# Optimization experiments

Measured on AMD Instinct MI355X. Metric: run time of the kernel, lower is better.

The kernel has to match this reference:

```python
import jax, jax.numpy as jnp
import numpy as np

B, N, D, H, HD = 4, 2048, 512, 8, 64
FF = 1024
C2, HF, WF = 128, 64, 64
EPS = 1e-6


def setup_inputs() -> dict:
    key = jax.random.key(0)
    ks = jax.random.split(key, 9)
    def nrm(k, shape, s=0.02):
        return jax.random.normal(k, shape, dtype=jnp.float32) * s
    x = jax.random.normal(ks[0], (B, N, D), dtype=jnp.float32)
    theta = jax.random.normal(ks[1], (B, H, N, HD // 2), dtype=jnp.float32)
    fmaps = jax.random.normal(ks[2], (B, C2, HF, WF), dtype=jnp.float32)
    # pixel-unit (x, y) coords in [0, W-1] / [0, H-1]
    coords = jax.random.uniform(ks[3], (B, N, 2), dtype=jnp.float32) * (WF - 1)
    return dict(
        x=x, theta=theta, fmaps=fmaps, coords=coords,
        w_corr=nrm(ks[4], (D, C2)),
        norm1_scale=jnp.ones((D,), jnp.float32),
        qk_scale_q=jnp.ones((HD,), jnp.float32),
        qk_scale_k=jnp.ones((HD,), jnp.float32),
        w_qkv=nrm(ks[5], (3 * D, D)),
        w_out=nrm(ks[6], (D, D)),
        norm2_scale=jnp.ones((D,), jnp.float32),
        w_ff1=nrm(ks[7], (2 * FF, D)),
        b_ff1=jnp.zeros((2 * FF,), jnp.float32),
        w_ff2=nrm(ks[8], (D, FF)),
    )


def rms_norm(x, scale, eps=EPS):
    ms = jnp.mean(jnp.square(x), axis=-1, keepdims=True)
    return x * (scale * jax.lax.rsqrt(ms + eps))


def apply_rotary(x, theta):
    # rotates first 2*d channels of the head dim, as in _apply_rotary_emb_inplace
    d = theta.shape[-1]
    x1, x2 = x[..., :d], x[..., d:2 * d]
    cos, sin = jnp.cos(theta), jnp.sin(theta)
    y1 = x1 * cos - x2 * sin
    y2 = x2 * cos + x1 * sin
    return jnp.concatenate([y1, y2, x[..., 2 * d:]], axis=-1)


def bilinear_sample(fmaps, coords):
    # fmaps [B,C,H,W], coords [B,N,2] (x,y) pixels; border padding, align_corners=True
    Hh, Ww = fmaps.shape[-2], fmaps.shape[-1]
    xc = jnp.clip(coords[..., 0], 0.0, Ww - 1.0)
    yc = jnp.clip(coords[..., 1], 0.0, Hh - 1.0)
    x0 = jnp.floor(xc); y0 = jnp.floor(yc)
    wx = xc - x0; wy = yc - y0
    x0i = x0.astype(jnp.int32); x1i = jnp.minimum(x0i + 1, Ww - 1)
    y0i = y0.astype(jnp.int32); y1i = jnp.minimum(y0i + 1, Hh - 1)
    def gather_one(img, yi, xi):  # img [C,H,W] -> [C,N]
        return img[:, yi, xi]
    g = jax.vmap(gather_one)
    f00 = g(fmaps, y0i, x0i); f01 = g(fmaps, y0i, x1i)
    f10 = g(fmaps, y1i, x0i); f11 = g(fmaps, y1i, x1i)
    wx = wx[:, None, :]; wy = wy[:, None, :]
    top = f00 * (1.0 - wx) + f01 * wx
    bot = f10 * (1.0 - wx) + f11 * wx
    out = top * (1.0 - wy) + bot * wy  # [B,C,N]
    return jnp.transpose(out, (0, 2, 1))  # [B,N,C]


def reference(x, theta, fmaps, coords, w_corr, norm1_scale, qk_scale_q,
              qk_scale_k, w_qkv, w_out, norm2_scale, w_ff1, b_ff1, w_ff2):
    # correlation features injected into tokens
    feats = bilinear_sample(fmaps, coords)          # [B,N,C2]
    x = x + feats @ w_corr.T                        # [B,N,D]
    # --- attention block (pre-RMSNorm, qk-norm, RoPE, unscaled dot-product attn) ---
    skip = x
    xn = rms_norm(x, norm1_scale)
    qkv = xn @ w_qkv.T                              # [B,N,3D]
    q, k, v = jnp.split(qkv, 3, axis=-1)
    def to_heads(t):
        return jnp.transpose(t.reshape(t.shape[0], t.shape[1], H, HD), (0, 2, 1, 3))
    q, k, v = to_heads(q), to_heads(k), to_heads(v)  # [B,H,N,HD]
    q = rms_norm(q, qk_scale_q)
    k = rms_norm(k, qk_scale_k)
    q = apply_rotary(q, theta)
    k = apply_rotary(k, theta)
    # dot_product_attn: raw q @ k^T (no 1/sqrt(d)), softmax, @ v
    attn = jax.nn.softmax(jnp.einsum('bhid,bhjd->bhij', q, k), axis=-1)
    o = jnp.einsum('bhij,bhjd->bhid', attn, v)
    o = jnp.transpose(o, (0, 2, 1, 3)).reshape(x.shape[0], x.shape[1], D)
    x = skip + o @ w_out.T
    # --- feedforward block (GEGLU) ---
    skip = x
    xn = rms_norm(x, norm2_scale)
    h = xn @ w_ff1.T + b_ff1
    hx, gate = jnp.split(h, 2, axis=-1)
    h = hx * jax.nn.gelu(gate, approximate=False)
    return skip + h @ w_ff2.T
```

## Files before the change

### kernel.cpp

```cpp
#include <hip/hip_runtime.h>
#include <hip/hip_bf16.h>
#include <math.h>

#define Bsz 4
#define Nseq 2048
#define Dm 512
#define Hn 8
#define HDm 64
#define FFm 1024
#define Cc 128
#define EPSf 1e-6f

typedef __attribute__((ext_vector_type(8))) short short8;
typedef __attribute__((ext_vector_type(4))) float f32x4;
typedef __attribute__((ext_vector_type(16))) float f32x16;
typedef __attribute__((ext_vector_type(4))) unsigned u32x4;

#define AS1(p) ((__attribute__((address_space(1))) void*)((void*)(p)))
#define AS3(p) ((__attribute__((address_space(3))) void*)(p))

__device__ __forceinline__ float bf2f(unsigned short u) {
    return __uint_as_float(((unsigned)u) << 16);
}
__device__ __forceinline__ unsigned short f2bf(float f) {
    unsigned u = __float_as_uint(f);
    return (unsigned short)((u + 0x7fffu + ((u >> 16) & 1u)) >> 16);
}
__device__ __forceinline__ unsigned cvt_pk_bf16(float lo, float hi) {
    unsigned r;
    asm("v_cvt_pk_bf16_f32 %0, %1, %2" : "=v"(r) : "v"(lo), "v"(hi));
    return r;
}
__device__ __forceinline__ bool is_f32(const unsigned* dtp) {
    return dtp[0] == 0x3F800000u;
}

#define LOG2E 1.4426950408889634f
#define SHIFT2 92.33248261689366f

#define CONV_TOTAL 2690176
__global__ __launch_bounds__(256) void convert_kernel(
    const void* s0, const void* s1, const void* s2, const void* s3,
    const void* s4, const void* s5, const void* s6, const void* s7,
    const void* s8, const void* s9,
    unsigned short* __restrict__ canon, const unsigned* __restrict__ dtp)
{
    int i = blockIdx.x * 256 + threadIdx.x;
    if (i >= CONV_TOTAL) return;
    const void* src; int j;
    if      (i < 786432)  { src = s0; j = i; }
    else if (i < 1835008) { src = s1; j = i - 786432; }
    else if (i < 2359296) { src = s2; j = i - 1835008; }
    else if (i < 2621440) { src = s3; j = i - 2359296; }
    else if (i < 2686976) { src = s4; j = i - 2621440; }
    else if (i < 2689024) { src = s5; j = i - 2686976; }
    else if (i < 2689536) { src = s6; j = i - 2689024; }
    else if (i < 2690048) { src = s7; j = i - 2689536; }
    else if (i < 2690112) { src = s8; j = i - 2690048; }
    else                  { src = s9; j = i - 2690112; }
    canon[i] = is_f32(dtp) ? f2bf(((const float*)src)[j])
                           : ((const unsigned short*)src)[j];
}

__global__ __launch_bounds__(256) void sample_kernel(
    const void* __restrict__ fmaps,
    const void* __restrict__ coords,
    unsigned short* __restrict__ feats,
    const unsigned* __restrict__ dtp)
{
    const bool f32m = is_f32(dtp);
    int i = blockIdx.x * 256 + threadIdx.x;
    int t = i >> 7;
    int c = i & 127;
    int b = t >> 11;
    float xc, yc;
    if (f32m) { xc = ((const float*)coords)[2 * t];  yc = ((const float*)coords)[2 * t + 1]; }
    else      { xc = bf2f(((const unsigned short*)coords)[2 * t]);
                yc = bf2f(((const unsigned short*)coords)[2 * t + 1]); }
    xc = fminf(fmaxf(xc, 0.f), 63.f);
    yc = fminf(fmaxf(yc, 0.f), 63.f);
    float x0f = floorf(xc), y0f = floorf(yc);
    float wx = xc - x0f, wy = yc - y0f;
    int x0 = (int)x0f, y0 = (int)y0f;
    int x1 = min(x0 + 1, 63), y1 = min(y0 + 1, 63);
    size_t fb = ((size_t)b * Cc + c) << 12;
    float f00, f01, f10, f11;
    if (f32m) {
        const float* fp = (const float*)fmaps + fb;
        f00 = fp[(y0 << 6) + x0]; f01 = fp[(y0 << 6) + x1];
        f10 = fp[(y1 << 6) + x0]; f11 = fp[(y1 << 6) + x1];
    } else {
        const unsigned short* fp = (const unsigned short*)fmaps + fb;
        f00 = bf2f(fp[(y0 << 6) + x0]); f01 = bf2f(fp[(y0 << 6) + x1]);
        f10 = bf2f(fp[(y1 << 6) + x0]); f11 = bf2f(fp[(y1 << 6) + x1]);
    }
    float top = f00 * (1.f - wx) + f01 * wx;
    float bot = f10 * (1.f - wx) + f11 * wx;
    feats[i] = f2bf(top * (1.f - wy) + bot * wy);
}

template<int BN>
__global__ __launch_bounds__(256, 4) void gemm_bt(
    const unsigned short* __restrict__ A,
    const unsigned short* __restrict__ W,
    const unsigned short* __restrict__ bias,
    const float* __restrict__ resF,
    const void* __restrict__ resRaw,
    float* __restrict__ outF,
    unsigned short* __restrict__ outB,
    void* __restrict__ outRaw,
    const unsigned* __restrict__ dtp,
    int M, int N, int K)
{
    constexpr int NT = BN / 32;
    __shared__ __align__(16) unsigned short As[2][128 * 32];
    __shared__ __align__(16) unsigned short Bs[2][BN * 32];
    const int tid = threadIdx.x;
    const int wave = tid >> 6, lane = tid & 63;
    const int quad = lane >> 4, l16 = lane & 15;
    const int wm = wave >> 1, wn = wave & 1;
    const int rowBase = blockIdx.y * 128;
    const int colBase = blockIdx.x * BN;
    const unsigned short* Ab = A + (size_t)rowBase * K;
    const unsigned short* Wb = W + (size_t)colBase * K;
    const int sr = lane >> 2;
    const int sc = (lane & 3) * 8;

    f32x4 acc[4][NT] = {};

    auto stage = [&](int buf, int k0) {
#pragma unroll
        for (int c = 0; c < 2; ++c) {
            int chunk = wave + c * 4;
            const unsigned short* ga = Ab + (size_t)(chunk * 16 + sr) * K + k0 + sc;
            __builtin_amdgcn_global_load_lds(AS1(ga), AS3(&As[buf][chunk * 512]), 16, 0, 0);
        }
#pragma unroll
        for (int c = 0; c < BN / 16; c += 4) {
            int chunk = wave + c;
            const unsigned short* gb = Wb + (size_t)(chunk * 16 + sr) * K + k0 + sc;
            __builtin_amdgcn_global_load_lds(AS1(gb), AS3(&Bs[buf][chunk * 512]), 16, 0, 0);
        }
    };

    const int nk = K >> 5;
    stage(0, 0);
    for (int kt = 0; kt < nk; ++kt) {
        const int buf = kt & 1;
        __syncthreads();
        __builtin_amdgcn_sched_barrier(0);
        if (kt + 1 < nk) stage(1 - buf, (kt + 1) << 5);
        short8 af[4], bfr[NT];
#pragma unroll
        for (int mt = 0; mt < 4; ++mt)
            af[mt] = *(const short8*)&As[buf][(wm * 64 + mt * 16 + l16) * 32 + quad * 8];
#pragma unroll
        for (int nt = 0; nt < NT; ++nt)
            bfr[nt] = *(const short8*)&Bs[buf][(wn * (BN / 2) + nt * 16 + l16) * 32 + quad * 8];
        __builtin_amdgcn_s_setprio(1);
#pragma unroll
        for (int mt = 0; mt < 4; ++mt)
#pragma unroll
            for (int nt = 0; nt < NT; ++nt)
                acc[mt][nt] = __builtin_amdgcn_mfma_f32_16x16x32_bf16(
                    af[mt], bfr[nt], acc[mt][nt], 0, 0, 0);
        __builtin_amdgcn_s_setprio(0);
    }

    const bool f32m = dtp ? is_f32(dtp) : false;
#pragma unroll
    for (int mt = 0; mt < 4; ++mt) {
#pragma unroll
        for (int r = 0; r < 4; ++r) {
            int row = rowBase + wm * 64 + mt * 16 + quad * 4 + r;
            size_t rowoff = (size_t)row * N;
#pragma unroll
            for (int nt = 0; nt < NT; ++nt) {
                int col = colBase + wn * (BN / 2) + nt * 16 + l16;
                float v = acc[mt][nt][r];
                if (bias) v += bf2f(bias[col]);
                size_t idx = rowoff + col;
                if (resF) v += resF[idx];
                if (resRaw) v += f32m ? ((const float*)resRaw)[idx]
                                      : bf2f(((const unsigned short*)resRaw)[idx]);
                if (outF)      outF[idx] = v;
                else if (outB) outB[idx] = f2bf(v);
                else if (f32m) ((float*)outRaw)[idx] = v;
                else           ((unsigned short*)outRaw)[idx] = f2bf(v);
            }
        }
    }
}

__global__ __launch_bounds__(256) void rmsnorm_kernel(
    const float* __restrict__ X, const unsigned short* __restrict__ scale,
    unsigned short* __restrict__ Y)
{
    int t = blockIdx.x;
    int tid = threadIdx.x;
    const float* xr = X + (size_t)t * 512;
    float a = xr[tid], b = xr[tid + 256];
    float ss = a * a + b * b;
#pragma unroll
    for (int off = 1; off < 64; off <<= 1) ss += __shfl_xor(ss, off);
    __shared__ float red[4];
    int wave = tid >> 6, lane = tid & 63;
    if (lane == 0) red[wave] = ss;
    __syncthreads();
    float tot = red[0] + red[1] + red[2] + red[3];
    float r = rsqrtf(tot * (1.f / 512.f) + EPSf);
    Y[(size_t)t * 512 + tid]       = f2bf(a * (bf2f(scale[tid]) * r));
    Y[(size_t)t * 512 + tid + 256] = f2bf(b * (bf2f(scale[tid + 256]) * r));
}

__global__ __launch_bounds__(256) void qkv_rope_kernel(
    const unsigned short* __restrict__ qkv, const void* __restrict__ theta,
    const unsigned short* __restrict__ sq, const unsigned short* __restrict__ sk,
    unsigned short* __restrict__ Qo, unsigned short* __restrict__ Ko,
    const unsigned* __restrict__ dtp)
{
    const bool f32m = is_f32(dtp);
    int t = blockIdx.x;
    int b = t >> 11, n = t & 2047;
    int wave = threadIdx.x >> 6, lane = threadIdx.x & 63;
    const unsigned short* base = qkv + (size_t)t * 1536;
#pragma unroll
    for (int hh = 0; hh < 2; ++hh) {
        int h = wave + hh * 4;
        float q = bf2f(base[h * 64 + lane]);
        float k = bf2f(base[512 + h * 64 + lane]);
        float ssq = q * q, ssk = k * k;
#pragma unroll
        for (int off = 1; off < 64; off <<= 1) {
            ssq += __shfl_xor(ssq, off);
            ssk += __shfl_xor(ssk, off);
        }
        float qn = q * (bf2f(sq[lane]) * rsqrtf(ssq * (1.f / 64.f) + EPSf));
        float kn = k * (bf2f(sk[lane]) * rsqrtf(ssk * (1.f / 64.f) + EPSf));
        size_t thIdx = ((size_t)(b * Hn + h) * Nseq + n) * 32 + (lane & 31);
        float th = f32m ? ((const float*)theta)[thIdx]
                        : bf2f(((const unsigned short*)theta)[thIdx]);
        float cth = __cosf(th), sth = __sinf(th);
        float qp = __shfl_xor(qn, 32);
        float kp = __shfl_xor(kn, 32);
        float sgn = (lane < 32) ? -1.f : 1.f;
        float qr = qn * cth + sgn * qp * sth;
        float kr = kn * cth + sgn * kp * sth;
        size_t o = ((size_t)(b * Hn + h) * Nseq + n) * 64 + lane;
        Qo[o] = f2bf(qr * LOG2E);
        Ko[o] = f2bf(kr);
    }
}

__global__ __launch_bounds__(256) void vtrans_kernel(
    const unsigned short* __restrict__ qkvb, unsigned short* __restrict__ Vt)
{
    int bh = blockIdx.y;
    int b = bh >> 3, h = bh & 7;
    int tid = threadIdx.x;
    int d = tid & 63;
    int chunk = blockIdx.x * 4 + (tid >> 6);
    int n0 = chunk * 8;
    unsigned short v[8];
#pragma unroll
    for (int j = 0; j < 8; ++j)
        v[j] = qkvb[((size_t)(b * Nseq + n0 + j)) * 1536 + 1024 + h * 64 + d];
    *(short8*)&Vt[((size_t)bh * 64 + d) * Nseq + n0] = *(short8*)v;
}

__global__ __launch_bounds__(256, 4) void attn_kernel(
    const unsigned short* __restrict__ Qg,
    const unsigned short* __restrict__ Kg,
    const unsigned short* __restrict__ Vtg,
    float* __restrict__ Op,
    float* __restrict__ Lp)
{
    const int bh = blockIdx.x;
    const int b = bh >> 3, h = bh & 7;
    const int q0 = blockIdx.y * 128;
    const int kz = blockIdx.z;
    const int tid = threadIdx.x;
    const int wave = tid >> 6, lane = tid & 63;
    const int l31 = lane & 31, hh = lane >> 5;
    __shared__ __align__(16) unsigned short Ks[2][64 * 72];
    __shared__ __align__(16) unsigned short Vs[2][64 * 72];
    const size_t bhN = (size_t)bh * Nseq;

    short8 bq[4];
#pragma unroll
    for (int kc = 0; kc < 4; ++kc)
        bq[kc] = *(const short8*)&Qg[(bhN + q0 + wave * 32 + l31) * 64 + kc * 16 + hh * 8];

    f32x16 oa[2] = {};
    float lsum = 0.f;
    const int r8 = tid >> 3;
    const int c8e = (tid & 7) * 8;
    const unsigned short* kgb = Kg + bhN * 64;
    const unsigned short* vbase = Vtg + (size_t)bh * 64 * Nseq;
    const bool hi = (hh == 1);

    const int KT0 = kz * (Nseq / 128);
    const int KT1 = KT0 + (Nseq / 128);
    const int kb0 = KT0 * 64;

    short8 kr0 = *(const short8*)&kgb[(size_t)(kb0 + r8) * 64 + c8e];
    short8 kr1 = *(const short8*)&kgb[(size_t)(kb0 + r8 + 32) * 64 + c8e];
    short8 vr0 = *(const short8*)&vbase[(size_t)r8 * Nseq + kb0 + c8e];
    short8 vr1 = *(const short8*)&vbase[(size_t)(r8 + 32) * Nseq + kb0 + c8e];

    for (int kt = KT0; kt < KT1; ++kt) {
        const int cur = kt & 1;
        *(short8*)&Ks[cur][r8 * 72 + c8e]        = kr0;
        *(short8*)&Ks[cur][(r8 + 32) * 72 + c8e] = kr1;
        *(short8*)&Vs[cur][r8 * 72 + c8e]        = vr0;
        *(short8*)&Vs[cur][(r8 + 32) * 72 + c8e] = vr1;
        __syncthreads();
        __builtin_amdgcn_sched_barrier(0);
        if (kt + 1 < KT1) {
            const int kb = (kt + 1) * 64;
            kr0 = *(const short8*)&kgb[(size_t)(kb + r8) * 64 + c8e];
            kr1 = *(const short8*)&kgb[(size_t)(kb + r8 + 32) * 64 + c8e];
            vr0 = *(const short8*)&vbase[(size_t)r8 * Nseq + kb + c8e];
            vr1 = *(const short8*)&vbase[(size_t)(r8 + 32) * Nseq + kb + c8e];
        }

        f32x16 st[2];
#pragma unroll
        for (int mt = 0; mt < 2; ++mt)
#pragma unroll
            for (int e = 0; e < 16; ++e) st[mt][e] = -SHIFT2;
        __builtin_amdgcn_s_setprio(1);
#pragma unroll
        for (int kc = 0; kc < 4; ++kc) {
            short8 ak0 = *(const short8*)&Ks[cur][(l31) * 72 + kc * 16 + hh * 8];
            short8 ak1 = *(const short8*)&Ks[cur][(32 + l31) * 72 + kc * 16 + hh * 8];
            st[0] = __builtin_amdgcn_mfma_f32_32x32x16_bf16(ak0, bq[kc], st[0], 0, 0, 0);
            st[1] = __builtin_amdgcn_mfma_f32_32x32x16_bf16(ak1, bq[kc], st[1], 0, 0, 0);
        }
        __builtin_amdgcn_s_setprio(0);

        unsigned pk[2][8];
        float partial = 0.f;
#pragma unroll
        for (int t = 0; t < 2; ++t)
#pragma unroll
            for (int p = 0; p < 4; ++p) {
                float v0 = __builtin_amdgcn_exp2f(st[t][4 * p + 0]);
                float v1 = __builtin_amdgcn_exp2f(st[t][4 * p + 1]);
                float v2 = __builtin_amdgcn_exp2f(st[t][4 * p + 2]);
                float v3 = __builtin_amdgcn_exp2f(st[t][4 * p + 3]);
                partial += (v0 + v1) + (v2 + v3);
                pk[t][2 * p + 0] = cvt_pk_bf16(v0, v1);
                pk[t][2 * p + 1] = cvt_pk_bf16(v2, v3);
            }
        lsum += partial + __shfl_xor(partial, 32);

        __builtin_amdgcn_s_setprio(1);
#pragma unroll
        for (int kc = 0; kc < 4; ++kc) {
            const int tau = kc >> 1;
            const int pA = 2 * (kc & 1);
            const int pB = pA + 1;
            unsigned dA0 = pk[tau][2 * pA], dA1 = pk[tau][2 * pA + 1];
            unsigned dB0 = pk[tau][2 * pB], dB1 = pk[tau][2 * pB + 1];
            unsigned s0 = hi ? dA0 : dB0, s1 = hi ? dA1 : dB1;
            unsigned r0 = __shfl_xor(s0, 32), r1 = __shfl_xor(s1, 32);
            unsigned o0 = hi ? dB0 : dA0, o1 = hi ? dB1 : dA1;
            u32x4 av = { hi ? r0 : o0, hi ? r1 : o1,
                         hi ? o0 : r0, hi ? o1 : r1 };
            short8 ap = __builtin_bit_cast(short8, av);
            short8 bv0 = *(const short8*)&Vs[cur][(l31) * 72 + kc * 16 + hh * 8];
            short8 bv1 = *(const short8*)&Vs[cur][(32 + l31) * 72 + kc * 16 + hh * 8];
            oa[0] = __builtin_amdgcn_mfma_f32_32x32x16_bf16(ap, bv0, oa[0], 0, 0, 0);
            oa[1] = __builtin_amdgcn_mfma_f32_32x32x16_bf16(ap, bv1, oa[1], 0, 0, 0);
        }
        __builtin_amdgcn_s_setprio(0);
    }

    if (!hi)
        Lp[((size_t)kz * 32 + bh) * Nseq + q0 + wave * 32 + l31] = lsum;
    const size_t obase = (size_t)kz * (Bsz * Nseq);
#pragma unroll
    for (int nt = 0; nt < 2; ++nt)
#pragma unroll
        for (int i = 0; i < 16; ++i) {
            int qr = q0 + wave * 32 + (i & 3) + 8 * (i >> 2) + 4 * hh;
            Op[(obase + (size_t)b * Nseq + qr) * Dm + h * 64 + nt * 32 + l31] =
                oa[nt][i];
        }
}

__global__ __launch_bounds__(256) void attn_combine_kernel(
    const float* __restrict__ Op,
    const float* __restrict__ Lp,
    unsigned short* __restrict__ Og)
{
    int gid = blockIdx.x * 256 + threadIdx.x;
    size_t base = (size_t)gid * 8;
    int t = gid >> 6;
    int c = (gid & 63) * 8;
    int h = c >> 6;
    int bh = ((t >> 11) << 3) + h;
    int n = t & 2047;
    float l = Lp[(size_t)bh * Nseq + n] + Lp[(size_t)(32 * Nseq) + (size_t)bh * Nseq + n];
    float inv = 1.f / l;
    f32x4 a0 = *(const f32x4*)&Op[base];
    f32x4 a1 = *(const f32x4*)&Op[base + 4];
    f32x4 b0 = *(const f32x4*)&Op[(size_t)8192 * 512 + base];
    f32x4 b1 = *(const f32x4*)&Op[(size_t)8192 * 512 + base + 4];
    unsigned short o[8];
#pragma unroll
    for (int j = 0; j < 4; ++j) {
        o[j]     = f2bf((a0[j] + b0[j]) * inv);
        o[4 + j] = f2bf((a1[j] + b1[j]) * inv);
    }
    *(short8*)&Og[base] = *(short8*)o;
}

__global__ __launch_bounds__(256) void gate_kernel(
    const unsigned short* __restrict__ Hin, unsigned short* __restrict__ Hout)
{
    int i = blockIdx.x * 256 + threadIdx.x;
    int t = i >> 10, j = i & 1023;
    float hx = bf2f(Hin[(size_t)t * 2048 + j]);
    float g  = bf2f(Hin[(size_t)t * 2048 + 1024 + j]);
    float gl = 0.5f * g * (1.f + erff(g * 0.70710678118654752f));
    Hout[i] = f2bf(hx * gl);
}

extern "C" void kernel_launch(void* const* d_in, const int* in_sizes, int n_in,
                              void* d_out, int out_size, void* d_ws, size_t ws_size,
                              hipStream_t stream) {
    const void* x      = d_in[0];
    const void* theta  = d_in[1];
    const void* fmaps  = d_in[2];
    const void* coords = d_in[3];
    const void* w_corr = d_in[4];
    const void* n1s    = d_in[5];
    const void* sq     = d_in[6];
    const void* sk     = d_in[7];
    const void* w_qkv  = d_in[8];
    const void* w_out  = d_in[9];
    const void* n2s    = d_in[10];
    const void* w_ff1  = d_in[11];
    const void* b_ff1  = d_in[12];
    const void* w_ff2  = d_in[13];
    const unsigned* dtp = (const unsigned*)n1s;

    char* ws = (char*)d_ws;
    float*          x1    = (float*)(ws + 0);
    float*          x2    = (float*)(ws + 16777216);
    unsigned short* xn    = (unsigned short*)(ws + 33554432);
    unsigned short* qkvb  = (unsigned short*)(ws + 41943040);
    unsigned short* feats = (unsigned short*)(ws + 41943040);
    unsigned short* qb    = (unsigned short*)(ws + 67108864);
    unsigned short* kb    = (unsigned short*)(ws + 75497472);
    unsigned short* vt    = (unsigned short*)(ws + 83886080);
    unsigned short* ob    = (unsigned short*)(ws + 92274688);
    unsigned short* ff1o  = (unsigned short*)(ws + 41943040);
    unsigned short* hbuf  = (unsigned short*)(ws + 75497472);
    unsigned short* canon = (unsigned short*)(ws + 100663296);
    float*          opart = (float*)(ws + 16777216);
    float*          lpart = (float*)(ws + 50331648);
    unsigned short* wqkvc  = canon + 0;
    unsigned short* wff1c  = canon + 786432;
    unsigned short* wff2c  = canon + 1835008;
    unsigned short* woutc  = canon + 2359296;
    unsigned short* wcorrc = canon + 2621440;
    unsigned short* bff1c  = canon + 2686976;
    unsigned short* n1c    = canon + 2689024;
    unsigned short* n2c    = canon + 2689536;
    unsigned short* sqc    = canon + 2690048;
    unsigned short* skc    = canon + 2690112;

    convert_kernel<<<(CONV_TOTAL + 255) / 256, 256, 0, stream>>>(
        w_qkv, w_ff1, w_ff2, w_out, w_corr, b_ff1, n1s, n2s, sq, sk, canon, dtp);
    sample_kernel<<<4096, 256, 0, stream>>>(fmaps, coords, feats, dtp);
    gemm_bt<64><<<dim3(8, 64), 256, 0, stream>>>(feats, wcorrc, nullptr, nullptr, x,
                                                 x1, nullptr, nullptr, dtp, 8192, 512, 128);
    rmsnorm_kernel<<<8192, 256, 0, stream>>>(x1, n1c, xn);
    gemm_bt<128><<<dim3(12, 64), 256, 0, stream>>>(xn, wqkvc, nullptr, nullptr, nullptr,
                                                   nullptr, qkvb, nullptr, nullptr, 8192, 1536, 512);
    qkv_rope_kernel<<<8192, 256, 0, stream>>>(qkvb, theta, sqc, skc, qb, kb, dtp);
    vtrans_kernel<<<dim3(64, 32), 256, 0, stream>>>(qkvb, vt);
    attn_kernel<<<dim3(32, 16, 2), 256, 0, stream>>>(qb, kb, vt, opart, lpart);
    attn_combine_kernel<<<2048, 256, 0, stream>>>(opart, lpart, ob);
    gemm_bt<64><<<dim3(8, 64), 256, 0, stream>>>(ob, woutc, nullptr, x1, nullptr,
                                                 x2, nullptr, nullptr, nullptr, 8192, 512, 512);
    rmsnorm_kernel<<<8192, 256, 0, stream>>>(x2, n2c, xn);
    gemm_bt<128><<<dim3(16, 64), 256, 0, stream>>>(xn, wff1c, bff1c, nullptr, nullptr,
                                                   nullptr, ff1o, nullptr, nullptr, 8192, 2048, 512);
    gate_kernel<<<32768, 256, 0, stream>>>(ff1o, hbuf);
    gemm_bt<64><<<dim3(8, 64), 256, 0, stream>>>(hbuf, wff2c, nullptr, x2, nullptr,
                                                 nullptr, nullptr, d_out, dtp, 8192, 512, 1024);
}
```

Measured before the change: 363.9 us.

## Fuse GEGLU gate into FF1 GEMM epilogue via interleaved weight rows

```diff
diff --git a/kernel.cpp b/kernel.cpp
--- a/kernel.cpp
+++ b/kernel.cpp
@@ -49,11 +49,22 @@
     if (i >= CONV_TOTAL) return;
     const void* src; int j;
     if      (i < 786432)  { src = s0; j = i; }
-    else if (i < 1835008) { src = s1; j = i - 786432; }
+    else if (i < 1835008) {
+        src = s1;
+        int j0 = i - 786432;
+        int rr = j0 >> 9, cc = j0 & 511;
+        int q = rr >> 4, tt = rr & 15;
+        j = ((q & 1) * 1024 + (q >> 1) * 16 + tt) * 512 + cc;
+    }
     else if (i < 2359296) { src = s2; j = i - 1835008; }
     else if (i < 2621440) { src = s3; j = i - 2359296; }
     else if (i < 2686976) { src = s4; j = i - 2621440; }
-    else if (i < 2689024) { src = s5; j = i - 2686976; }
+    else if (i < 2689024) {
+        src = s5;
+        int j0 = i - 2686976;
+        int q = j0 >> 4, tt = j0 & 15;
+        j = (q & 1) * 1024 + (q >> 1) * 16 + tt;
+    }
     else if (i < 2689536) { src = s6; j = i - 2689024; }
     else if (i < 2690048) { src = s7; j = i - 2689536; }
     else if (i < 2690112) { src = s8; j = i - 2690048; }
@@ -109,6 +120,7 @@
     float* __restrict__ outF,
     unsigned short* __restrict__ outB,
     void* __restrict__ outRaw,
+    unsigned short* __restrict__ outG,
     const unsigned* __restrict__ dtp,
     int M, int N, int K)
 {
@@ -167,6 +179,24 @@
         __builtin_amdgcn_s_setprio(0);
     }
 
+    if (outG) {
+#pragma unroll
+        for (int mt = 0; mt < 4; ++mt)
+#pragma unroll
+            for (int r = 0; r < 4; ++r) {
+                int row = rowBase + wm * 64 + mt * 16 + quad * 4 + r;
+#pragma unroll
+                for (int nt = 0; nt < NT; nt += 2) {
+                    int colh = colBase + wn * (BN / 2) + nt * 16 + l16;
+                    float hx = acc[mt][nt][r]     + bf2f(bias[colh]);
+                    float g  = acc[mt][nt + 1][r] + bf2f(bias[colh + 16]);
+                    float gl = 0.5f * g * (1.f + erff(g * 0.70710678118654752f));
+                    int pc = (colBase >> 1) + wn * (BN / 4) + (nt >> 1) * 16 + l16;
+                    outG[(size_t)row * FFm + pc] = f2bf(hx * gl);
+                }
+            }
+        return;
+    }
     const bool f32m = dtp ? is_f32(dtp) : false;
 #pragma unroll
     for (int mt = 0; mt < 4; ++mt) {
@@ -415,17 +445,6 @@
         o[4 + j] = f2bf((a1[j] + b1[j]) * inv);
     }
     *(short8*)&Og[base] = *(short8*)o;
-}
-
-__global__ __launch_bounds__(256) void gate_kernel(
-    const unsigned short* __restrict__ Hin, unsigned short* __restrict__ Hout)
-{
-    int i = blockIdx.x * 256 + threadIdx.x;
-    int t = i >> 10, j = i & 1023;
-    float hx = bf2f(Hin[(size_t)t * 2048 + j]);
-    float g  = bf2f(Hin[(size_t)t * 2048 + 1024 + j]);
-    float gl = 0.5f * g * (1.f + erff(g * 0.70710678118654752f));
-    Hout[i] = f2bf(hx * gl);
 }
 
 extern "C" void kernel_launch(void* const* d_in, const int* in_sizes, int n_in,
@@ -457,7 +476,6 @@
     unsigned short* kb    = (unsigned short*)(ws + 75497472);
     unsigned short* vt    = (unsigned short*)(ws + 83886080);
     unsigned short* ob    = (unsigned short*)(ws + 92274688);
-    unsigned short* ff1o  = (unsigned short*)(ws + 41943040);
     unsigned short* hbuf  = (unsigned short*)(ws + 75497472);
     unsigned short* canon = (unsigned short*)(ws + 100663296);
     float*          opart = (float*)(ws + 16777216);
@@ -477,20 +495,19 @@
         w_qkv, w_ff1, w_ff2, w_out, w_corr, b_ff1, n1s, n2s, sq, sk, canon, dtp);
     sample_kernel<<<4096, 256, 0, stream>>>(fmaps, coords, feats, dtp);
     gemm_bt<64><<<dim3(8, 64), 256, 0, stream>>>(feats, wcorrc, nullptr, nullptr, x,
-                                                 x1, nullptr, nullptr, dtp, 8192, 512, 128);
+                                                 x1, nullptr, nullptr, nullptr, dtp, 8192, 512, 128);
     rmsnorm_kernel<<<8192, 256, 0, stream>>>(x1, n1c, xn);
     gemm_bt<128><<<dim3(12, 64), 256, 0, stream>>>(xn, wqkvc, nullptr, nullptr, nullptr,
-                                                   nullptr, qkvb, nullptr, nullptr, 8192, 1536, 512);
+                                                   nullptr, qkvb, nullptr, nullptr, nullptr, 8192, 1536, 512);
     qkv_rope_kernel<<<8192, 256, 0, stream>>>(qkvb, theta, sqc, skc, qb, kb, dtp);
     vtrans_kernel<<<dim3(64, 32), 256, 0, stream>>>(qkvb, vt);
     attn_kernel<<<dim3(32, 16, 2), 256, 0, stream>>>(qb, kb, vt, opart, lpart);
     attn_combine_kernel<<<2048, 256, 0, stream>>>(opart, lpart, ob);
     gemm_bt<64><<<dim3(8, 64), 256, 0, stream>>>(ob, woutc, nullptr, x1, nullptr,
-                                                 x2, nullptr, nullptr, nullptr, 8192, 512, 512);
+                                                 x2, nullptr, nullptr, nullptr, nullptr, 8192, 512, 512);
     rmsnorm_kernel<<<8192, 256, 0, stream>>>(x2, n2c, xn);
     gemm_bt<128><<<dim3(16, 64), 256, 0, stream>>>(xn, wff1c, bff1c, nullptr, nullptr,
-                                                   nullptr, ff1o, nullptr, nullptr, 8192, 2048, 512);
-    gate_kernel<<<32768, 256, 0, stream>>>(ff1o, hbuf);
+                                                   nullptr, nullptr, nullptr, hbuf, nullptr, 8192, 2048, 512);
     gemm_bt<64><<<dim3(8, 64), 256, 0, stream>>>(hbuf, wff2c, nullptr, x2, nullptr,
-                                                 nullptr, nullptr, d_out, dtp, 8192, 512, 1024);
-}
+                                                 nullptr, nullptr, d_out, nullptr, dtp, 8192, 512, 1024);
+}
```

Measured after the change: 338.0 us. 1.08x faster.
